# Kernel optimization log

Measured on AMD Instinct MI355X. Metric: run time of the kernel, lower is better.

Reference implementation:

```python
import jax, jax.numpy as jnp
import numpy as np

B, L, D = 128, 196, 1024  # batch, att_size, rnn_size


def setup_inputs() -> dict:
    key = jax.random.key(0)
    ks = jax.random.split(key, 11)
    s = 1.0 / np.sqrt(D)
    return {
        "x": jax.random.normal(ks[0], (B, D), jnp.float32),
        "att": jax.random.normal(ks[1], (B, L, D), jnp.float32),
        "h": jax.random.normal(ks[2], (B, D), jnp.float32),
        "W_a2a": jax.random.uniform(ks[3], (D, D), jnp.float32, -s, s),
        "b_a2a": jax.random.uniform(ks[4], (D,), jnp.float32, -s, s),
        "W_h2a": jax.random.uniform(ks[5], (D, D), jnp.float32, -s, s),
        "b_h2a": jax.random.uniform(ks[6], (D,), jnp.float32, -s, s),
        "W_i2a": jax.random.uniform(ks[7], (D, D), jnp.float32, -s, s),
        "b_i2a": jax.random.uniform(ks[8], (D,), jnp.float32, -s, s),
        "W_d2d": jax.random.uniform(ks[9], (D,), jnp.float32, -s, s),
        "b_d2d": jax.random.uniform(ks[10], (), jnp.float32, -s, s),
    }


def reference(x, att, h, W_a2a, b_a2a, W_h2a, b_h2a, W_i2a, b_i2a, W_d2d, b_d2d):
    # att_v_1: [B, L, D]
    att_v = jnp.einsum('bld,ed->ble', att, W_a2a) + b_a2a
    att_h = (h @ W_h2a.T + b_h2a)[:, None, :]   # [B, 1, D]
    att_x = (x @ W_i2a.T + b_i2a)[:, None, :]   # [B, 1, D]
    dot = jnp.tanh(att_v + att_h + att_x)       # [B, L, D]
    scores = jnp.einsum('bld,d->bl', dot, W_d2d) + b_d2d  # [B, L]
    weight = jax.nn.softmax(scores, axis=-1)    # [B, L]
    att_res = jnp.einsum('bld,bl->bd', att, weight)  # [B, D]
    return att_res
```

## Files before the change

### kernel.cpp

```cpp
#include <hip/hip_runtime.h>
#include <hip/hip_bf16.h>

#define B_ 128
#define L_ 196
#define D_ 1024

typedef __attribute__((ext_vector_type(8))) short short8v;
typedef __attribute__((ext_vector_type(4))) float f32x4;
typedef unsigned short ushort_t;

#define OFF_ATTBF   0UL
#define OFF_WBF     51380224UL
#define OFF_A2      53477376UL
#define OFF_W2      54001664UL
#define OFF_SPART   53477376UL
#define OFF_CPART   58195968UL

__device__ inline unsigned short f2bf(float f) {
  unsigned int u = __float_as_uint(f);
  unsigned int r = (u + 0x7fffu + ((u >> 16) & 1u)) >> 16;
  return (unsigned short)r;
}

__global__ void convert_kernel(const float* __restrict__ att, const float* __restrict__ Wa,
                               const float* __restrict__ x,   const float* __restrict__ h,
                               const float* __restrict__ Wi,  const float* __restrict__ Wh,
                               ushort_t* __restrict__ att_bf, ushort_t* __restrict__ W_bf,
                               ushort_t* __restrict__ A2,     ushort_t* __restrict__ W2) {
  const int n0 = (B_*L_*D_)/4;
  const int n1 = (D_*D_)/4;
  const int n2 = (B_*D_)/4;
  const int total = n0 + n1 + 2*n2 + 2*n1;
  for (int idx = blockIdx.x*blockDim.x + threadIdx.x; idx < total;
       idx += gridDim.x*blockDim.x) {
    const float4* src; ushort_t* dst;
    int i = idx;
    if (i < n0)               { src = (const float4*)att + i; dst = att_bf + (size_t)i*4; }
    else if ((i -= n0) < n1)  { src = (const float4*)Wa  + i; dst = W_bf  + (size_t)i*4; }
    else if ((i -= n1) < n2)  { int b = i>>8, k4 = i&255; src = (const float4*)x  + i; dst = A2 + b*2048 + k4*4; }
    else if ((i -= n2) < n2)  { int b = i>>8, k4 = i&255; src = (const float4*)h  + i; dst = A2 + b*2048 + 1024 + k4*4; }
    else if ((i -= n2) < n1)  { int e = i>>8, k4 = i&255; src = (const float4*)Wi + i; dst = W2 + e*2048 + k4*4; }
    else { i -= n1;             int e = i>>8, k4 = i&255; src = (const float4*)Wh + i; dst = W2 + e*2048 + 1024 + k4*4; }
    float4 v = *src;
    ushort4 o; o.x = f2bf(v.x); o.y = f2bf(v.y); o.z = f2bf(v.z); o.w = f2bf(v.w);
    *(ushort4*)dst = o;
  }
}

__device__ inline void stage_tile(const ushort_t* __restrict__ g, int row0, int Kld, int k0,
                                  ushort_t* ldst, int t) {
  #pragma unroll
  for (int it = 0; it < 4; ++it) {
    int linear = it*4096 + t*16;
    int r = linear >> 7;
    int c = (t & 7) ^ (r & 7);
    const ushort_t* src = g + (size_t)(row0 + r)*Kld + k0 + c*8;
    ushort_t* dst = ldst + ((it*4096 + ((t & 192) << 4)) >> 1);
    __builtin_amdgcn_global_load_lds((const __attribute__((address_space(1))) void*)src,
                                     (__attribute__((address_space(3))) void*)dst,
                                     16, 0, 0);
  }
}

__device__ inline short8v ldfrag(const ushort_t* tile, int row, int c) {
  int phys = c ^ (row & 7);
  return *(const short8v*)(tile + row*64 + phys*8);
}

__global__ __launch_bounds__(256) void gemm_c_kernel(
    const ushort_t* __restrict__ Amat, const ushort_t* __restrict__ Bmat,
    float* __restrict__ cpart) {
  __shared__ ushort_t lds[32768];
  int bid = blockIdx.x;
  int e0 = (bid & 7)*128;
  int kc = bid >> 3;
  int kbeg = kc*512;
  const int Kld = 2048;
  int t = threadIdx.x, lane = t & 63, w = t >> 6;
  int wm = w >> 1, we = w & 1;
  int lrow = lane & 15;
  int lk = lane >> 4;

  f32x4 acc[4][4];
  #pragma unroll
  for (int i = 0; i < 4; ++i)
    #pragma unroll
    for (int j = 0; j < 4; ++j) acc[i][j] = (f32x4){0.f, 0.f, 0.f, 0.f};

  stage_tile(Amat, 0,  Kld, kbeg, lds, t);
  stage_tile(Bmat, e0, Kld, kbeg, lds + 8192, t);
  __syncthreads();

  const int nk = 8;
  for (int kt = 0; kt < nk; ++kt) {
    int cur = kt & 1;
    if (kt + 1 < nk) {
      stage_tile(Amat, 0,  Kld, kbeg + ((kt+1) << 6), lds + (cur^1)*16384, t);
      stage_tile(Bmat, e0, Kld, kbeg + ((kt+1) << 6), lds + (cur^1)*16384 + 8192, t);
    }
    const ushort_t* At = lds + cur*16384;
    const ushort_t* Bt = At + 8192;
    #pragma unroll
    for (int hh = 0; hh < 2; ++hh) {
      short8v af[4], bfv[4];
      #pragma unroll
      for (int i = 0; i < 4; ++i) af[i]  = ldfrag(At, wm*64 + i*16 + lrow, hh*4 + lk);
      #pragma unroll
      for (int j = 0; j < 4; ++j) bfv[j] = ldfrag(Bt, we*64 + j*16 + lrow, hh*4 + lk);
      #pragma unroll
      for (int i = 0; i < 4; ++i)
        #pragma unroll
        for (int j = 0; j < 4; ++j)
          acc[i][j] = __builtin_amdgcn_mfma_f32_16x16x32_bf16(af[i], bfv[j], acc[i][j], 0, 0, 0);
    }
    __syncthreads();
  }

  float* outc = cpart + (size_t)kc*131072;
  #pragma unroll
  for (int i = 0; i < 4; ++i) {
    int m = wm*64 + i*16 + lk*4;
    #pragma unroll
    for (int j = 0; j < 4; ++j) {
      int e = e0 + we*64 + j*16 + lrow;
      #pragma unroll
      for (int r = 0; r < 4; ++r)
        outc[(m + r)*1024 + e] = acc[i][j][r];
    }
  }
}

__device__ inline short8v ldfrag2(const ushort_t* tile, int row, int c) {
  int phys = c ^ (row & 7);
  return *(const short8v*)(tile + row*64 + phys*8);
}

#define STAGE(lanebase, half, kt, ldsT) { \
    const ushort_t* s0_ = (lanebase) + (half)*131072 + (kt)*64; \
    ushort_t* d0_ = (ldsT) + (half)*8192 + w*512; \
    __builtin_amdgcn_global_load_lds((const __attribute__((address_space(1))) void*)s0_, \
                                     (__attribute__((address_space(3))) void*)d0_, 16, 0, 0); \
    __builtin_amdgcn_global_load_lds((const __attribute__((address_space(1))) void*)(s0_ + 65536), \
                                     (__attribute__((address_space(3))) void*)(d0_ + 4096), 16, 0, 0); }

#define BARR()  __builtin_amdgcn_s_barrier()
#define VM8()   asm volatile("s_waitcnt vmcnt(8)" ::: "memory")

#define RD_ALO_K(base, kk) { _Pragma("unroll") for (int i_=0;i_<4;++i_) \
    aLo[i_][kk] = ldfrag2(base, wm*64 + i_*16 + lrow, (kk)*4 + lk); }
#define RD_AHI_K(base, kk) { _Pragma("unroll") for (int i_=0;i_<4;++i_) \
    aHi[i_][kk] = ldfrag2(base, 128 + wm*64 + i_*16 + lrow, (kk)*4 + lk); }
#define RD_B01_K(base, kk) { _Pragma("unroll") for (int j_=0;j_<2;++j_) \
    b01[j_][kk] = ldfrag2(base, wn*64 + j_*16 + lrow, (kk)*4 + lk); }
#define RD_B23_K(base, kk) { _Pragma("unroll") for (int j_=0;j_<2;++j_) \
    b23[j_][kk] = ldfrag2(base, wn*64 + (2+j_)*16 + lrow, (kk)*4 + lk); }

#define MQ(I0, J0, A_, B_) { _Pragma("unroll") for (int k_=0;k_<2;++k_) { \
    _Pragma("unroll") for (int i_=0;i_<4;++i_) { _Pragma("unroll") for (int j_=0;j_<2;++j_) { \
      acc[(I0)+i_][(J0)+j_] = __builtin_amdgcn_mfma_f32_16x16x32_bf16(A_[i_][k_], B_[j_][k_], acc[(I0)+i_][(J0)+j_], 0,0,0); } } } }

#define KTILE_BODY(Abuf, Bbuf) \
    RD_ALO_K(Abuf, 0); RD_B01_K(Bbuf, 0); RD_B23_K(Bbuf, 0); \
    RD_ALO_K(Abuf, 1); RD_B01_K(Bbuf, 1); RD_B23_K(Bbuf, 1); \
    MQ(0, 0, aLo, b01); \
    RD_AHI_K(Abuf, 0); RD_AHI_K(Abuf, 1); \
    MQ(0, 2, aLo, b23); \
    MQ(4, 0, aHi, b01); \
    MQ(4, 2, aHi, b23);

__global__ __launch_bounds__(512, 2) void gemm_score_kernel(
    const ushort_t* __restrict__ Amat, const ushort_t* __restrict__ Bmat,
    const float* __restrict__ cpart,
    const float* __restrict__ ba, const float* __restrict__ bh, const float* __restrict__ bi,
    const float* __restrict__ wd,
    float* __restrict__ spart) {
  __shared__ ushort_t lds[65536];
  __shared__ float c_lds[768];
  const int nk = 16;
  int bid = blockIdx.x;
  int swz = (bid & 7)*49 + (bid >> 3);
  int m_blk = swz >> 2, e_blk = swz & 3;
  int m0 = m_blk*256, e0 = e_blk*256;
  int t = (int)threadIdx.x, lane = t & 63, w = t >> 6;
  int wm = w >> 2, wn = w & 3;
  int lrow = lane & 15, lk = lane >> 4;

  int bb0 = m0 / 196;
  for (int idx = t; idx < 768; idx += 512) {
    int bb = bb0 + (idx >> 8);
    int e  = e0 + (idx & 255);
    float v = ba[e] + bh[e] + bi[e];
    if (bb < 128) {
      v += cpart[bb*1024 + e] + cpart[131072 + bb*1024 + e]
         + cpart[262144 + bb*1024 + e] + cpart[393216 + bb*1024 + e];
    }
    c_lds[idx] = v;
  }

  int r0 = t >> 3;
  int c0 = (t & 7) ^ (r0 & 7);
  const ushort_t* aBase = Amat + (size_t)(m0 + r0)*1024 + c0*8;
  const ushort_t* bBase = Bmat + (size_t)(e0 + r0)*1024 + c0*8;

  ushort_t* A0_ = lds;
  ushort_t* B0_ = lds + 16384;
  ushort_t* A1_ = lds + 32768;
  ushort_t* B1_ = lds + 49152;

  f32x4 acc[8][4];
  #pragma unroll
  for (int i = 0; i < 8; ++i)
    #pragma unroll
    for (int j = 0; j < 4; ++j) acc[i][j] = (f32x4){0.f, 0.f, 0.f, 0.f};
  short8v aLo[4][2], aHi[4][2], b01[2][2], b23[2][2];

  STAGE(aBase, 0, 0, A0_); STAGE(aBase, 1, 0, A0_);
  STAGE(bBase, 0, 0, B0_); STAGE(bBase, 1, 0, B0_);
  STAGE(aBase, 0, 1, A1_); STAGE(aBase, 1, 1, A1_);
  STAGE(bBase, 0, 1, B1_); STAGE(bBase, 1, 1, B1_);

  for (int it2 = 0; it2 < 8; ++it2) {
    int kt = 2*it2;
    VM8();
    BARR();
    KTILE_BODY(A0_, B0_);
    BARR();
    { int ks = (kt+2 < nk) ? kt+2 : nk-1;
      STAGE(aBase, 0, ks, A0_); STAGE(aBase, 1, ks, A0_);
      STAGE(bBase, 0, ks, B0_); STAGE(bBase, 1, ks, B0_); }
    VM8();
    BARR();
    KTILE_BODY(A1_, B1_);
    BARR();
    { int ks = (kt+3 < nk) ? kt+3 : nk-1;
      STAGE(aBase, 0, ks, A1_); STAGE(aBase, 1, ks, A1_);
      STAGE(bBase, 0, ks, B1_); STAGE(bBase, 1, ks, B1_); }
  }

  int p = e_blk*4 + wn;
  #pragma unroll
  for (int i = 0; i < 8; ++i) {
    int mbase = m0 + (i>>2)*128 + wm*64 + (i&3)*16 + lk*4;
    f32x4 ps;
    #pragma unroll
    for (int r = 0; r < 4; ++r) {
      int m = mbase + r;
      int bb = (int)((unsigned)m / 196u);
      float partial = 0.f;
      #pragma unroll
      for (int j = 0; j < 4; ++j) {
        int ee = wn*64 + j*16 + lrow;
        float v = acc[i][j][r] + c_lds[(bb - bb0)*256 + ee];
        float ex = __expf(2.f*v);
        partial += (1.f - 2.f/(ex + 1.f)) * wd[e0 + ee];
      }
      partial += __shfl_xor(partial, 1);
      partial += __shfl_xor(partial, 2);
      partial += __shfl_xor(partial, 4);
      partial += __shfl_xor(partial, 8);
      ps[r] = partial;
    }
    if (lrow == 0) *(f32x4*)(spart + (size_t)p*25088 + mbase) = ps;
  }
}

__global__ __launch_bounds__(256) void finalize_kernel(const ushort_t* __restrict__ att_bf,
                                                       const float* __restrict__ spart,
                                                       float* __restrict__ out) {
  int b  = blockIdx.x >> 1;
  int dh = blockIdx.x & 1;
  int t  = threadIdx.x;
  __shared__ float wls[L_];
  __shared__ float red[8];

  float s = -1e30f;
  if (t < L_) {
    int m = b*L_ + t;
    float sum = 0.f;
    #pragma unroll
    for (int p = 0; p < 16; ++p) sum += spart[p*25088 + m];
    s = sum;
  }
  float mx = s;
  #pragma unroll
  for (int off = 1; off < 64; off <<= 1) mx = fmaxf(mx, __shfl_xor(mx, off));
  if ((t & 63) == 0) red[t >> 6] = mx;
  __syncthreads();
  mx = fmaxf(fmaxf(red[0], red[1]), fmaxf(red[2], red[3]));
  float pr = (t < L_) ? __expf(s - mx) : 0.f;
  float ssum = pr;
  #pragma unroll
  for (int off = 1; off < 64; off <<= 1) ssum += __shfl_xor(ssum, off);
  if ((t & 63) == 0) red[4 + (t >> 6)] = ssum;
  __syncthreads();
  float tot = red[4] + red[5] + red[6] + red[7];
  if (t < L_) wls[t] = pr / tot;
  __syncthreads();

  int d = dh*512 + t*2;
  const ushort_t* abase = att_bf + (size_t)b*L_*D_ + d;
  float a0 = 0.f, a1 = 0.f;
  #pragma unroll 4
  for (int l = 0; l < L_; ++l) {
    float wv = wls[l];
    unsigned int v = *(const unsigned int*)(abase + (size_t)l*D_);
    float lo = __uint_as_float(v << 16);
    float hi = __uint_as_float(v & 0xffff0000u);
    a0 += wv*lo; a1 += wv*hi;
  }
  float2 o; o.x = a0; o.y = a1;
  *(float2*)(out + (size_t)b*D_ + d) = o;
}

extern "C" void kernel_launch(void* const* d_in, const int* in_sizes, int n_in,
                              void* d_out, int out_size, void* d_ws, size_t ws_size,
                              hipStream_t stream) {
  (void)in_sizes; (void)n_in; (void)out_size; (void)ws_size;
  const float* x   = (const float*)d_in[0];
  const float* att = (const float*)d_in[1];
  const float* h   = (const float*)d_in[2];
  const float* Wa  = (const float*)d_in[3];
  const float* ba  = (const float*)d_in[4];
  const float* Wh  = (const float*)d_in[5];
  const float* bh  = (const float*)d_in[6];
  const float* Wi  = (const float*)d_in[7];
  const float* bi  = (const float*)d_in[8];
  const float* wd  = (const float*)d_in[9];

  char* ws = (char*)d_ws;
  ushort_t* att_bf = (ushort_t*)(ws + OFF_ATTBF);
  ushort_t* W_bf   = (ushort_t*)(ws + OFF_WBF);
  ushort_t* A2     = (ushort_t*)(ws + OFF_A2);
  ushort_t* W2     = (ushort_t*)(ws + OFF_W2);
  float*    cpart  = (float*)(ws + OFF_CPART);
  float*    spart  = (float*)(ws + OFF_SPART);
  float*    out    = (float*)d_out;

  hipLaunchKernelGGL(convert_kernel, dim3(2048), dim3(256), 0, stream,
                     att, Wa, x, h, Wi, Wh, att_bf, W_bf, A2, W2);
  hipLaunchKernelGGL(gemm_c_kernel, dim3(32), dim3(256), 0, stream,
                     A2, W2, cpart);
  hipLaunchKernelGGL(gemm_score_kernel, dim3(392), dim3(512), 0, stream,
                     att_bf, W_bf, cpart, ba, bh, bi, wd, spart);
  hipLaunchKernelGGL(finalize_kernel, dim3(256), dim3(256), 0, stream,
                     att_bf, spart, out);
}
```

Measured before the change: 126.2 us.

## Shrink score GEMM tiles to 128x128 with single-buffered LDS and more blocks

The fused score GEMM moves from 256x256 tiles with 512 threads and double-buffered LDS to 128x128 tiles with 256 threads, a single LDS buffer and a full vmcnt(0) wait each k-step. The grid grows from 392 to 1568 blocks. Smaller LDS and register footprints should let more blocks share each CU, hiding latency through occupancy rather than software pipelining. The MFMA section is raised with s_setprio. In exchange, each operand is re-read from L2 more often, and loads no longer overlap compute within a block.

```diff
diff --git a/kernel.cpp b/kernel.cpp
--- a/kernel.cpp
+++ b/kernel.cpp
@@ -130,117 +130,100 @@
   }
 }
 
-__device__ inline short8v ldfrag2(const ushort_t* tile, int row, int c) {
-  int phys = c ^ (row & 7);
-  return *(const short8v*)(tile + row*64 + phys*8);
-}
-
-#define STAGE(lanebase, half, kt, ldsT) { \
-    const ushort_t* s0_ = (lanebase) + (half)*131072 + (kt)*64; \
-    ushort_t* d0_ = (ldsT) + (half)*8192 + w*512; \
-    __builtin_amdgcn_global_load_lds((const __attribute__((address_space(1))) void*)s0_, \
-                                     (__attribute__((address_space(3))) void*)d0_, 16, 0, 0); \
-    __builtin_amdgcn_global_load_lds((const __attribute__((address_space(1))) void*)(s0_ + 65536), \
-                                     (__attribute__((address_space(3))) void*)(d0_ + 4096), 16, 0, 0); }
-
 #define BARR()  __builtin_amdgcn_s_barrier()
-#define VM8()   asm volatile("s_waitcnt vmcnt(8)" ::: "memory")
-
-#define RD_ALO_K(base, kk) { _Pragma("unroll") for (int i_=0;i_<4;++i_) \
-    aLo[i_][kk] = ldfrag2(base, wm*64 + i_*16 + lrow, (kk)*4 + lk); }
-#define RD_AHI_K(base, kk) { _Pragma("unroll") for (int i_=0;i_<4;++i_) \
-    aHi[i_][kk] = ldfrag2(base, 128 + wm*64 + i_*16 + lrow, (kk)*4 + lk); }
-#define RD_B01_K(base, kk) { _Pragma("unroll") for (int j_=0;j_<2;++j_) \
-    b01[j_][kk] = ldfrag2(base, wn*64 + j_*16 + lrow, (kk)*4 + lk); }
-#define RD_B23_K(base, kk) { _Pragma("unroll") for (int j_=0;j_<2;++j_) \
-    b23[j_][kk] = ldfrag2(base, wn*64 + (2+j_)*16 + lrow, (kk)*4 + lk); }
-
-#define MQ(I0, J0, A_, B_) { _Pragma("unroll") for (int k_=0;k_<2;++k_) { \
-    _Pragma("unroll") for (int i_=0;i_<4;++i_) { _Pragma("unroll") for (int j_=0;j_<2;++j_) { \
-      acc[(I0)+i_][(J0)+j_] = __builtin_amdgcn_mfma_f32_16x16x32_bf16(A_[i_][k_], B_[j_][k_], acc[(I0)+i_][(J0)+j_], 0,0,0); } } } }
-
-#define KTILE_BODY(Abuf, Bbuf) \
-    RD_ALO_K(Abuf, 0); RD_B01_K(Bbuf, 0); RD_B23_K(Bbuf, 0); \
-    RD_ALO_K(Abuf, 1); RD_B01_K(Bbuf, 1); RD_B23_K(Bbuf, 1); \
-    MQ(0, 0, aLo, b01); \
-    RD_AHI_K(Abuf, 0); RD_AHI_K(Abuf, 1); \
-    MQ(0, 2, aLo, b23); \
-    MQ(4, 0, aHi, b01); \
-    MQ(4, 2, aHi, b23);
-
-__global__ __launch_bounds__(512, 2) void gemm_score_kernel(
+#define VM0()   asm volatile("s_waitcnt vmcnt(0)" ::: "memory")
+
+__device__ inline void stageS(const ushort_t* __restrict__ g, int k0, ushort_t* ldsbase, int t) {
+  #pragma unroll
+  for (int it = 0; it < 4; ++it) {
+    int linear = it*4096 + t*16;
+    int r = linear >> 7;
+    int c = ((linear >> 4) & 7) ^ (r & 7);
+    const ushort_t* src = g + (size_t)r*1024 + k0 + c*8;
+    ushort_t* dst = ldsbase + ((it*4096 + ((t & 192) << 4)) >> 1);
+    __builtin_amdgcn_global_load_lds((const __attribute__((address_space(1))) void*)src,
+                                     (__attribute__((address_space(3))) void*)dst,
+                                     16, 0, 0);
+  }
+}
+
+__global__ __launch_bounds__(256) void gemm_score_kernel(
     const ushort_t* __restrict__ Amat, const ushort_t* __restrict__ Bmat,
     const float* __restrict__ cpart,
     const float* __restrict__ ba, const float* __restrict__ bh, const float* __restrict__ bi,
     const float* __restrict__ wd,
     float* __restrict__ spart) {
-  __shared__ ushort_t lds[65536];
-  __shared__ float c_lds[768];
-  const int nk = 16;
+  __shared__ ushort_t lds[16384];
+  __shared__ float c_lds[256];
   int bid = blockIdx.x;
-  int swz = (bid & 7)*49 + (bid >> 3);
-  int m_blk = swz >> 2, e_blk = swz & 3;
-  int m0 = m_blk*256, e0 = e_blk*256;
+  int swz = (bid & 7)*196 + (bid >> 3);
+  int m_blk = swz >> 3, n_blk = swz & 7;
+  int m0 = m_blk*128, e0 = n_blk*128;
   int t = (int)threadIdx.x, lane = t & 63, w = t >> 6;
-  int wm = w >> 2, wn = w & 3;
+  int wm = w >> 1, we = w & 1;
   int lrow = lane & 15, lk = lane >> 4;
 
   int bb0 = m0 / 196;
-  for (int idx = t; idx < 768; idx += 512) {
-    int bb = bb0 + (idx >> 8);
-    int e  = e0 + (idx & 255);
+  {
+    int bb = bb0 + (t >> 7);
+    int e  = e0 + (t & 127);
     float v = ba[e] + bh[e] + bi[e];
     if (bb < 128) {
       v += cpart[bb*1024 + e] + cpart[131072 + bb*1024 + e]
          + cpart[262144 + bb*1024 + e] + cpart[393216 + bb*1024 + e];
     }
-    c_lds[idx] = v;
-  }
-
-  int r0 = t >> 3;
-  int c0 = (t & 7) ^ (r0 & 7);
-  const ushort_t* aBase = Amat + (size_t)(m0 + r0)*1024 + c0*8;
-  const ushort_t* bBase = Bmat + (size_t)(e0 + r0)*1024 + c0*8;
-
-  ushort_t* A0_ = lds;
-  ushort_t* B0_ = lds + 16384;
-  ushort_t* A1_ = lds + 32768;
-  ushort_t* B1_ = lds + 49152;
-
-  f32x4 acc[8][4];
-  #pragma unroll
-  for (int i = 0; i < 8; ++i)
+    c_lds[t] = v;
+  }
+
+  const ushort_t* aG = Amat + (size_t)m0*1024;
+  const ushort_t* bG = Bmat + (size_t)e0*1024;
+
+  int lrow7 = lrow & 7;
+  const ushort_t* pA0 = lds + (wm*64 + lrow)*64 + ((lk)     ^ lrow7)*8;
+  const ushort_t* pA1 = lds + (wm*64 + lrow)*64 + (((4+lk)) ^ lrow7)*8;
+  const ushort_t* pB0 = lds + 8192 + (we*64 + lrow)*64 + ((lk)     ^ lrow7)*8;
+  const ushort_t* pB1 = lds + 8192 + (we*64 + lrow)*64 + (((4+lk)) ^ lrow7)*8;
+
+  f32x4 acc[4][4];
+  #pragma unroll
+  for (int i = 0; i < 4; ++i)
     #pragma unroll
     for (int j = 0; j < 4; ++j) acc[i][j] = (f32x4){0.f, 0.f, 0.f, 0.f};
-  short8v aLo[4][2], aHi[4][2], b01[2][2], b23[2][2];
-
-  STAGE(aBase, 0, 0, A0_); STAGE(aBase, 1, 0, A0_);
-  STAGE(bBase, 0, 0, B0_); STAGE(bBase, 1, 0, B0_);
-  STAGE(aBase, 0, 1, A1_); STAGE(aBase, 1, 1, A1_);
-  STAGE(bBase, 0, 1, B1_); STAGE(bBase, 1, 1, B1_);
-
-  for (int it2 = 0; it2 < 8; ++it2) {
-    int kt = 2*it2;
-    VM8();
+
+  stageS(aG, 0, lds, t);
+  stageS(bG, 0, lds + 8192, t);
+
+  for (int kt = 0; kt < 16; ++kt) {
+    VM0();
     BARR();
-    KTILE_BODY(A0_, B0_);
+    __builtin_amdgcn_s_setprio(1);
+    #pragma unroll
+    for (int ks = 0; ks < 2; ++ks) {
+      const ushort_t* pa = ks ? pA1 : pA0;
+      const ushort_t* pb = ks ? pB1 : pB0;
+      short8v af[4], bfv[4];
+      #pragma unroll
+      for (int i = 0; i < 4; ++i) af[i]  = *(const short8v*)(pa + i*1024);
+      #pragma unroll
+      for (int j = 0; j < 4; ++j) bfv[j] = *(const short8v*)(pb + j*1024);
+      #pragma unroll
+      for (int i = 0; i < 4; ++i)
+        #pragma unroll
+        for (int j = 0; j < 4; ++j)
+          acc[i][j] = __builtin_amdgcn_mfma_f32_16x16x32_bf16(af[i], bfv[j], acc[i][j], 0, 0, 0);
+    }
+    __builtin_amdgcn_s_setprio(0);
     BARR();
-    { int ks = (kt+2 < nk) ? kt+2 : nk-1;
-      STAGE(aBase, 0, ks, A0_); STAGE(aBase, 1, ks, A0_);
-      STAGE(bBase, 0, ks, B0_); STAGE(bBase, 1, ks, B0_); }
-    VM8();
-    BARR();
-    KTILE_BODY(A1_, B1_);
-    BARR();
-    { int ks = (kt+3 < nk) ? kt+3 : nk-1;
-      STAGE(aBase, 0, ks, A1_); STAGE(aBase, 1, ks, A1_);
-      STAGE(bBase, 0, ks, B1_); STAGE(bBase, 1, ks, B1_); }
-  }
-
-  int p = e_blk*4 + wn;
-  #pragma unroll
-  for (int i = 0; i < 8; ++i) {
-    int mbase = m0 + (i>>2)*128 + wm*64 + (i&3)*16 + lk*4;
+    if (kt < 15) {
+      stageS(aG, (kt+1)*64, lds, t);
+      stageS(bG, (kt+1)*64, lds + 8192, t);
+    }
+  }
+
+  int p = n_blk*2 + we;
+  #pragma unroll
+  for (int i = 0; i < 4; ++i) {
+    int mbase = m0 + wm*64 + i*16 + lk*4;
     f32x4 ps;
     #pragma unroll
     for (int r = 0; r < 4; ++r) {
@@ -249,8 +232,8 @@
       float partial = 0.f;
       #pragma unroll
       for (int j = 0; j < 4; ++j) {
-        int ee = wn*64 + j*16 + lrow;
-        float v = acc[i][j][r] + c_lds[(bb - bb0)*256 + ee];
+        int ee = we*64 + j*16 + lrow;
+        float v = acc[i][j][r] + c_lds[(bb - bb0)*128 + ee];
         float ex = __expf(2.f*v);
         partial += (1.f - 2.f/(ex + 1.f)) * wd[e0 + ee];
       }
@@ -340,7 +323,7 @@
                      att, Wa, x, h, Wi, Wh, att_bf, W_bf, A2, W2);
   hipLaunchKernelGGL(gemm_c_kernel, dim3(32), dim3(256), 0, stream,
                      A2, W2, cpart);
-  hipLaunchKernelGGL(gemm_score_kernel, dim3(392), dim3(512), 0, stream,
+  hipLaunchKernelGGL(gemm_score_kernel, dim3(1568), dim3(256), 0, stream,
                      att_bf, W_bf, cpart, ba, bh, bi, wd, spart);
   hipLaunchKernelGGL(finalize_kernel, dim3(256), dim3(256), 0, stream,
                      att_bf, spart, out);
```

Result: no change. 127.7 us (+1.2%).
